# Performance work log

Measured on AMD Instinct MI355X. Metric: run time of the kernel, lower is better.

## Reference

```python
import jax, jax.numpy as jnp
import numpy as np

B, T, N_EMBD, HEAD = 8, 2048, 1024, 64
NEG_INF = -1e30  # stand-in for float('-inf'), safe under fp16/bf16 after where


def setup_inputs() -> dict:
    key = jax.random.key(0)
    k0, k1, k2, k3 = jax.random.split(key, 4)
    idx = jax.random.normal(k0, (B, T, N_EMBD), dtype=jnp.float32)
    # nn.Linear weights have shape (out_features, in_features)
    Wk = jax.random.normal(k1, (HEAD, N_EMBD), dtype=jnp.float32) * 0.02
    Wq = jax.random.normal(k2, (HEAD, N_EMBD), dtype=jnp.float32) * 0.02
    Wv = jax.random.normal(k3, (HEAD, N_EMBD), dtype=jnp.float32) * 0.02
    return {"idx": idx, "Wk": Wk, "Wq": Wq, "Wv": Wv}


def reference(idx, Wk, Wq, Wv):
    # idx: [B,T,C]; W*: [H,C] (torch Linear layout, y = x @ W.T)
    Tn = idx.shape[1]
    k = jnp.einsum('btc,hc->bth', idx, Wk)
    q = jnp.einsum('btc,hc->bth', idx, Wq)
    v = jnp.einsum('btc,hc->bth', idx, Wv)
    # NOTE: original has NO 1/sqrt(head_size) scaling
    wei = jnp.einsum('bth,bsh->bts', q, k)  # [B,T,T]
    causal = jnp.tril(jnp.ones((Tn, Tn), dtype=bool))  # keep where tril != 0
    wei = jnp.where(causal[None, :, :], wei, NEG_INF)
    # NOTE: original softmaxes over dim=1 (query axis), not the last axis
    wei = jax.nn.softmax(wei, axis=1)
    out = jnp.einsum('bts,bsh->bth', wei, v)  # [B,T,H]
    return out
```

## Files before the change

### kernel.cpp

```cpp
#include <hip/hip_runtime.h>


typedef __attribute__((ext_vector_type(8))) short bf16x8;
typedef __attribute__((ext_vector_type(4))) float f32x4;
typedef unsigned short u16;

#define MFMA(a, b, c) __builtin_amdgcn_mfma_f32_16x16x32_bf16((a), (b), (c), 0, 0, 0)

__device__ __forceinline__ u16 f2bf(float x) {
    unsigned u = __float_as_uint(x);
    u += 0x7fff + ((u >> 16) & 1);
    return (u16)(u >> 16);
}
__device__ __forceinline__ float bf2f(u16 h) {
    return __uint_as_float(((unsigned)h) << 16);
}

__device__ __forceinline__ void split8(const f32x4 x0, const f32x4 x1,
                                       bf16x8* hv, bf16x8* lv)
{
    const float f[8] = {x0[0], x0[1], x0[2], x0[3], x1[0], x1[1], x1[2], x1[3]};
    union { unsigned u[4]; bf16x8 v; } H, L;
    #pragma unroll
    for (int j = 0; j < 4; ++j) {
        const unsigned u0 = __float_as_uint(f[2 * j]);
        const unsigned u1 = __float_as_uint(f[2 * j + 1]);
        H.u[j] = __builtin_amdgcn_perm(u1, u0, 0x07060302);
        const float l0 = f[2 * j]     - __uint_as_float(u0 & 0xffff0000u);
        const float l1 = f[2 * j + 1] - __uint_as_float(u1 & 0xffff0000u);
        L.u[j] = __builtin_amdgcn_perm(__float_as_uint(l1), __float_as_uint(l0),
                                       0x07060302);
    }
    *hv = H.v;
    *lv = L.v;
}

typedef const __attribute__((address_space(1))) void* gas_p;
typedef __attribute__((address_space(3))) void* las_p;

#define WH_OFF  0u
#define WL_OFF  (WH_OFF + 192u*1024u*2u)
#define FQH_OFF (WL_OFF + 192u*1024u*2u)
#define FQL_OFF (FQH_OFF + 2u*1024u*1024u)
#define FKH_OFF (FQL_OFF + 2u*1024u*1024u)
#define FKL_OFF (FKH_OFF + 2u*1024u*1024u)
#define VF_OFF  (FKL_OFF + 2u*1024u*1024u)
#define DD_OFF  (VF_OFF + 2u*1024u*1024u)
#define PF_OFF  (DD_OFF + 8u*2048u*4u)

__global__ __launch_bounds__(128) void wsplit_kernel(
    const float* __restrict__ Wk, const float* __restrict__ Wq,
    const float* __restrict__ Wv, u16* __restrict__ FWH)
{
    const int n = blockIdx.x;
    const int nblk = n >> 4, lr = n & 15;
    const float* src = (n < 64) ? (Wq + (long)n * 1024)
                     : (n < 128) ? (Wk + (long)(n - 64) * 1024)
                                 : (Wv + (long)(n - 128) * 1024);
    const int f = threadIdx.x;
    const int kc = f >> 2, q = f & 3;
    const float4 f0 = *(const float4*)&src[kc * 32 + q * 8];
    const float4 f1 = *(const float4*)&src[kc * 32 + q * 8 + 4];
    const float vs[8] = {f0.x, f0.y, f0.z, f0.w, f1.x, f1.y, f1.z, f1.w};
    bf16x8 hv;
    #pragma unroll
    for (int j = 0; j < 8; ++j) hv[j] = (short)f2bf(vs[j]);
    const long o = ((long)(nblk * 32 + kc) * 64 + q * 16 + lr) * 8;
    *(bf16x8*)&FWH[o] = hv;
}

__global__ __launch_bounds__(512, 2) void qkv_kernel(
    const float* __restrict__ idx, const u16* __restrict__ FWH,
    u16* __restrict__ FQH, u16* __restrict__ FQL,
    u16* __restrict__ FKH, u16* __restrict__ VF)
{
    __shared__ __align__(16) char smem[3][40960];
    const int tid = threadIdx.x;
    const int w = tid >> 6, lr = tid & 15, quad = (tid >> 4) & 3;
    const int lane = tid & 63;
    const int r0 = blockIdx.x * 64;
    const int b = r0 >> 11, t0 = r0 & 2047;
    const int m0 = (w & 1) * 32;
    const int nbb = (w >> 1) * 3;

    const float* asrc[2];
    int adst[2];
    #pragma unroll
    for (int j = 0; j < 2; ++j) {
        const int s = w * 2 + j;
        const int row = s * 4 + (lane >> 4);
        const int lc = (lane & 15) ^ (row & 7);
        asrc[j] = idx + (long)(r0 + row) * 1024 + lc * 4;
        adst[j] = s * 1024;
    }
    const u16* fsrc[3];
    int fdst[3];
    #pragma unroll
    for (int j = 0; j < 3; ++j) {
        const int seg = w * 3 + j;
        const int nblk = seg >> 1, kcl = seg & 1;
        fsrc[j] = FWH + (long)nblk * 16384 + kcl * 512 + lane * 8;
        fdst[j] = 16384 + seg * 1024;
    }

#define ISSUE(PH)                                                             \
    {                                                                         \
        const int nb_ = (PH) % 3;                                             \
        _Pragma("unroll")                                                     \
        for (int j = 0; j < 2; ++j)                                           \
            __builtin_amdgcn_global_load_lds((gas_p)(asrc[j] + (PH) * 64),    \
                (las_p)(smem[nb_] + adst[j]), 16, 0, 0);                      \
        _Pragma("unroll")                                                     \
        for (int j = 0; j < 3; ++j)                                           \
            __builtin_amdgcn_global_load_lds((gas_p)(fsrc[j] + (long)(PH) * 1024), \
                (las_p)(smem[nb_] + fdst[j]), 16, 0, 0);                      \
    }

#define COMPUTE(PH)                                                           \
    {                                                                         \
        const int nb_ = (PH) % 3;                                             \
        const float* A_ = (const float*)smem[nb_];                            \
        const u16* F_ = (const u16*)(smem[nb_] + 16384);                      \
        _Pragma("unroll")                                                     \
        for (int kc = 0; kc < 2; ++kc) {                                      \
            bf16x8 AH[2], AL[2];                                              \
            _Pragma("unroll")                                                 \
            for (int mi = 0; mi < 2; ++mi) {                                  \
                const int R = m0 + mi * 16 + lr;                              \
                const int c0 = (kc * 8 + quad * 2) ^ (lr & 7);                \
                const f32x4 x0 = *(const f32x4*)&A_[R * 64 + c0 * 4];         \
                const f32x4 x1 = *(const f32x4*)&A_[R * 64 + (c0 ^ 1) * 4];   \
                split8(x0, x1, &AH[mi], &AL[mi]);                             \
            }                                                                 \
            _Pragma("unroll")                                                 \
            for (int nf = 0; nf < 3; ++nf) {                                  \
                const int sb = (((nbb + nf) * 2 + kc)) * 512 + lane * 8;      \
                const bf16x8 bh = *(const bf16x8*)&F_[sb];                    \
                _Pragma("unroll")                                             \
                for (int mi = 0; mi < 2; ++mi) {                              \
                    f32x4 c = acc[mi][nf];                                    \
                    c = MFMA(AH[mi], bh, c);                                  \
                    c = MFMA(AL[mi], bh, c);                                  \
                    acc[mi][nf] = c;                                          \
                }                                                             \
            }                                                                 \
        }                                                                     \
    }

#define WAITV(N)                                                              \
    asm volatile("s_waitcnt vmcnt(" #N ")" ::: "memory");                     \
    __builtin_amdgcn_sched_barrier(0);                                        \
    __builtin_amdgcn_s_barrier();

    f32x4 acc[2][3] = {};

    ISSUE(0); ISSUE(1);
    WAITV(5)

    for (int ph = 0; ph < 14; ++ph) {
        ISSUE(ph + 2);
        __builtin_amdgcn_sched_barrier(0);
        COMPUTE(ph);
        WAITV(5)
    }
    COMPUTE(14);
    WAITV(0)
    COMPUTE(15);

#undef WAITV
#undef COMPUTE
#undef ISSUE

    #pragma unroll
    for (int mi = 0; mi < 2; ++mi) {
        const int tb = t0 + m0 + mi * 16 + quad * 4;
        const int tblk = (t0 + m0 + mi * 16) >> 4;
        #pragma unroll
        for (int nf = 0; nf < 3; ++nf) {
            const int n = (nbb + nf) * 16 + lr;
            const f32x4 a = acc[mi][nf];
            if (n < 128) {
                const bool isQ = (n < 64);
                const int h = n & 63;
                const int kc = h >> 5;
                const int lsub = 16 * ((h & 31) >> 3);
                const long base = ((long)(b * 128 + tblk) * 2 + kc) * 512 + (h & 7);
                #pragma unroll
                for (int r = 0; r < 4; ++r) {
                    const float v = a[r];
                    const u16 hi = f2bf(v);
                    const long o = base + (long)(quad * 4 + r + lsub) * 8;
                    if (isQ) {
                        FQH[o] = hi;
                        FQL[o] = f2bf(v - bf2f(hi));
                    } else {
                        FKH[o] = hi;
                    }
                }
            } else {
                const int h = n - 128;
                const int hblk = h >> 4;
                #pragma unroll
                for (int r = 0; r < 4; ++r) {
                    const int t = tb + r;
                    const long o = ((long)(b * 4 + hblk) * 64 + (t >> 5)) * 512
                                 + (long)(16 * ((t & 31) >> 3) + (h & 15)) * 8 + (t & 7);
                    VF[o] = f2bf(a[r]);
                }
            }
        }
    }
}

__global__ __launch_bounds__(256, 4) void stats_kernel(
    const u16* __restrict__ FQH, const u16* __restrict__ FQL,
    const u16* __restrict__ FKH,
    u16* __restrict__ PF, float* __restrict__ D)
{
    __shared__ float red[4][64];
    const int tid = threadIdx.x;
    const int w = tid >> 6, lr = tid & 15, quad = (tid >> 4) & 3;
    const int lane = tid & 63;
    const int b = blockIdx.y;
    int x = blockIdx.x, i = 0;
    for (;;) { const int nc = (39 - i) >> 3; if (x < nc) break; x -= nc; ++i; }
    const int s0 = i * 64;
    const int jt0 = i + 8 * x, jt1 = min(jt0 + 8, 32);

    uint2* __restrict__ PQ = (uint2*)PF;

    bf16x8 KH[4][2];
    #pragma unroll
    for (int sf = 0; sf < 4; ++sf) {
        const long kb = ((long)(b * 128 + i * 4 + sf) * 2) * 512 + lane * 8;
        KH[sf][0] = *(const bf16x8*)&FKH[kb];
        KH[sf][1] = *(const bf16x8*)&FKH[kb + 512];
    }

    float dsum[4][4] = {};
    for (int jt = jt0; jt < jt1; ++jt) {
        const long qb = ((long)(b * 128 + jt * 4 + w) * 2) * 512 + lane * 8;
        const bf16x8 qh0 = *(const bf16x8*)&FQH[qb];
        const bf16x8 qh1 = *(const bf16x8*)&FQH[qb + 512];
        const bf16x8 ql0 = *(const bf16x8*)&FQL[qb];
        const bf16x8 ql1 = *(const bf16x8*)&FQL[qb + 512];
        const bool diag = (jt == i);
        const int t_sub = w * 16 + lr;
        const long tb_base = ((long)(b * 128 + jt * 4 + w)) * 512;
        #pragma unroll
        for (int sf = 0; sf < 4; ++sf) {
            f32x4 cc = {};
            cc = MFMA(KH[sf][0], qh0, cc);
            cc = MFMA(KH[sf][0], ql0, cc);
            cc = MFMA(KH[sf][1], qh1, cc);
            cc = MFMA(KH[sf][1], ql1, cc);

            u16 hq[4];
            #pragma unroll
            for (int r = 0; r < 4; ++r) {
                float ev = __expf(cc[r]);
                if (diag && (t_sub < sf * 16 + quad * 4 + r)) ev = 0.f;
                dsum[sf][r] += ev;
                hq[r] = f2bf(ev);
            }
            uint2 pk;
            pk.x = (unsigned)hq[0] | ((unsigned)hq[1] << 16);
            pk.y = (unsigned)hq[2] | ((unsigned)hq[3] << 16);
            PQ[(tb_base + i * 16 + sf * 4 + quad) * 16 + lr] = pk;
        }
    }

    #pragma unroll
    for (int sf = 0; sf < 4; ++sf)
        #pragma unroll
        for (int r = 0; r < 4; ++r) {
            float v = dsum[sf][r];
            v += __shfl_xor(v, 1);
            v += __shfl_xor(v, 2);
            v += __shfl_xor(v, 4);
            v += __shfl_xor(v, 8);
            dsum[sf][r] = v;
        }
    if (lr == 0) {
        #pragma unroll
        for (int sf = 0; sf < 4; ++sf)
            #pragma unroll
            for (int r = 0; r < 4; ++r)
                red[w][sf * 16 + quad * 4 + r] = dsum[sf][r];
    }
    __syncthreads();
    if (tid < 64)
        atomicAdd(&D[b * 2048 + s0 + tid],
                  red[0][tid] + red[1][tid] + red[2][tid] + red[3][tid]);
}

__global__ __launch_bounds__(256) void vscale_kernel(
    u16* __restrict__ VF, const float* __restrict__ D)
{
    const int g = blockIdx.x * 256 + threadIdx.x;
    const long e = (long)g * 8;
    const int lane = (int)((e >> 3) & 63);
    const int kc   = (int)((e >> 9) & 63);
    const int b    = (int)(e >> 17);
    const int s = kc * 32 + (lane >> 4) * 8;
    const float4 d0 = *(const float4*)&D[b * 2048 + s];
    const float4 d1 = *(const float4*)&D[b * 2048 + s + 4];
    const float dv[8] = {d0.x, d0.y, d0.z, d0.w, d1.x, d1.y, d1.z, d1.w};
    bf16x8 vv = *(bf16x8*)&VF[e];
    bf16x8 ov;
    #pragma unroll
    for (int j = 0; j < 8; ++j)
        ov[j] = (short)f2bf(bf2f((u16)vv[j]) / dv[j]);
    *(bf16x8*)&VF[e] = ov;
}

__global__ __launch_bounds__(256, 4) void out_kernel(
    const u16* __restrict__ PF, const u16* __restrict__ VF,
    float* __restrict__ out)
{
    const int tid = threadIdx.x;
    const int w = tid >> 6, lr = tid & 15, quad = (tid >> 4) & 3;
    const int lane = tid & 63;
    const int b = blockIdx.y;
    int x = blockIdx.x, i = 0;
    for (;;) { const int nc = (i + 8) >> 3; if (x < nc) break; x -= nc; ++i; }
    const int t0 = i * 64;
    const int js0 = 8 * x, js1 = min(8 * x + 8, i + 1);
    const int tblk = i * 4 + w;

    const uint2* __restrict__ PQ = (const uint2*)PF;
    const int g = lane >> 4, tr = lane & 15;
    const long tb_base = ((long)(b * 128 + tblk)) * 512;

    f32x4 oacc[4] = {};
    for (int js = js0; js < js1; ++js) {
        bf16x8 pa[2];
        #pragma unroll
        for (int kcp = 0; kcp < 2; ++kcp) {
            const long u = (tb_base + js * 16 + kcp * 8 + g * 2) * 16 + tr;
            const uint2 a0 = PQ[u];
            const uint2 a1 = PQ[u + 16];
            union { unsigned uu[4]; bf16x8 v; } P_;
            P_.uu[0] = a0.x; P_.uu[1] = a0.y; P_.uu[2] = a1.x; P_.uu[3] = a1.y;
            pa[kcp] = P_.v;
        }
        #pragma unroll
        for (int nf = 0; nf < 4; ++nf) {
            const long vb = ((long)(b * 4 + nf) * 64 + 2 * js) * 512 + lane * 8;
            const bf16x8 v0 = *(const bf16x8*)&VF[vb];
            const bf16x8 v1 = *(const bf16x8*)&VF[vb + 512];
            oacc[nf] = MFMA(pa[0], v0, oacc[nf]);
            oacc[nf] = MFMA(pa[1], v1, oacc[nf]);
        }
    }

    const bool single = (i < 8);
    #pragma unroll
    for (int nf = 0; nf < 4; ++nf) {
        const int h = nf * 16 + lr;
        #pragma unroll
        for (int r = 0; r < 4; ++r) {
            const int t = t0 + w * 16 + quad * 4 + r;
            const long o = (long)(b * 2048 + t) * 64 + h;
            if (single) out[o] = oacc[nf][r];
            else        atomicAdd(&out[o], oacc[nf][r]);
        }
    }
}

extern "C" void kernel_launch(void* const* d_in, const int* in_sizes, int n_in,
                              void* d_out, int out_size, void* d_ws, size_t ws_size,
                              hipStream_t stream)
{
    const float* idx = (const float*)d_in[0];
    const float* Wk  = (const float*)d_in[1];
    const float* Wq  = (const float*)d_in[2];
    const float* Wv  = (const float*)d_in[3];
    char* ws = (char*)d_ws;
    float* out = (float*)d_out;

    u16* FWH = (u16*)(ws + WH_OFF);
    u16* FQH = (u16*)(ws + FQH_OFF); u16* FQL = (u16*)(ws + FQL_OFF);
    u16* FKH = (u16*)(ws + FKH_OFF);
    u16* VF  = (u16*)(ws + VF_OFF);
    float* Dp = (float*)(ws + DD_OFF);
    u16* PF  = (u16*)(ws + PF_OFF);

    hipMemsetAsync(out, 0, (size_t)8 * 2048 * 64 * sizeof(float), stream);
    hipMemsetAsync(Dp, 0, (size_t)8 * 2048 * sizeof(float), stream);

    wsplit_kernel<<<192, 128, 0, stream>>>(Wk, Wq, Wv, FWH);
    qkv_kernel<<<256, 512, 0, stream>>>(idx, FWH, FQH, FQL, FKH, VF);
    stats_kernel<<<dim3(80, 8), 256, 0, stream>>>(FQH, FQL, FKH, PF, Dp);
    vscale_kernel<<<512, 256, 0, stream>>>(VF, Dp);
    out_kernel<<<dim3(80, 8), 256, 0, stream>>>(PF, VF, out);
}
```

Measured before the change: 145.9 us.

## Drop Q low-part split and fold column-sum normalization into output kernel

Removes the hi/lo bf16 split of Q, so the score computation uses two MFMAs per tile instead of four and no longer writes or reads the FQL buffer. It also deletes the separate vscale kernel that divided V by the column sums. That division now happens in out_kernel, where each P element is multiplied by the reciprocal of its column sum before the MFMA. The intent is to save one kernel launch plus memory traffic and matrix work. In exchange, the scores lose precision because Q is now a single bf16 value, and with no 1/sqrt scaling the exponent amplifies that error, so accuracy may suffer. The normalization also uses an approximate reciprocal.

```diff
diff --git a/kernel.cpp b/kernel.cpp
--- a/kernel.cpp
+++ b/kernel.cpp
@@ -71,8 +71,7 @@
 
 __global__ __launch_bounds__(512, 2) void qkv_kernel(
     const float* __restrict__ idx, const u16* __restrict__ FWH,
-    u16* __restrict__ FQH, u16* __restrict__ FQL,
-    u16* __restrict__ FKH, u16* __restrict__ VF)
+    u16* __restrict__ FQH, u16* __restrict__ FKH, u16* __restrict__ VF)
 {
     __shared__ __align__(16) char smem[3][40960];
     const int tid = threadIdx.x;
@@ -180,22 +179,15 @@
             const int n = (nbb + nf) * 16 + lr;
             const f32x4 a = acc[mi][nf];
             if (n < 128) {
-                const bool isQ = (n < 64);
+                u16* Hd = (n < 64) ? FQH : FKH;
                 const int h = n & 63;
                 const int kc = h >> 5;
                 const int lsub = 16 * ((h & 31) >> 3);
                 const long base = ((long)(b * 128 + tblk) * 2 + kc) * 512 + (h & 7);
                 #pragma unroll
                 for (int r = 0; r < 4; ++r) {
-                    const float v = a[r];
-                    const u16 hi = f2bf(v);
                     const long o = base + (long)(quad * 4 + r + lsub) * 8;
-                    if (isQ) {
-                        FQH[o] = hi;
-                        FQL[o] = f2bf(v - bf2f(hi));
-                    } else {
-                        FKH[o] = hi;
-                    }
+                    Hd[o] = f2bf(a[r]);
                 }
             } else {
                 const int h = n - 128;
@@ -213,8 +205,7 @@
 }
 
 __global__ __launch_bounds__(256, 4) void stats_kernel(
-    const u16* __restrict__ FQH, const u16* __restrict__ FQL,
-    const u16* __restrict__ FKH,
+    const u16* __restrict__ FQH, const u16* __restrict__ FKH,
     u16* __restrict__ PF, float* __restrict__ D)
 {
     __shared__ float red[4][64];
@@ -242,8 +233,6 @@
         const long qb = ((long)(b * 128 + jt * 4 + w) * 2) * 512 + lane * 8;
         const bf16x8 qh0 = *(const bf16x8*)&FQH[qb];
         const bf16x8 qh1 = *(const bf16x8*)&FQH[qb + 512];
-        const bf16x8 ql0 = *(const bf16x8*)&FQL[qb];
-        const bf16x8 ql1 = *(const bf16x8*)&FQL[qb + 512];
         const bool diag = (jt == i);
         const int t_sub = w * 16 + lr;
         const long tb_base = ((long)(b * 128 + jt * 4 + w)) * 512;
@@ -251,9 +240,7 @@
         for (int sf = 0; sf < 4; ++sf) {
             f32x4 cc = {};
             cc = MFMA(KH[sf][0], qh0, cc);
-            cc = MFMA(KH[sf][0], ql0, cc);
             cc = MFMA(KH[sf][1], qh1, cc);
-            cc = MFMA(KH[sf][1], ql1, cc);
 
             u16 hq[4];
             #pragma unroll
@@ -294,29 +281,9 @@
                   red[0][tid] + red[1][tid] + red[2][tid] + red[3][tid]);
 }
 
-__global__ __launch_bounds__(256) void vscale_kernel(
-    u16* __restrict__ VF, const float* __restrict__ D)
-{
-    const int g = blockIdx.x * 256 + threadIdx.x;
-    const long e = (long)g * 8;
-    const int lane = (int)((e >> 3) & 63);
-    const int kc   = (int)((e >> 9) & 63);
-    const int b    = (int)(e >> 17);
-    const int s = kc * 32 + (lane >> 4) * 8;
-    const float4 d0 = *(const float4*)&D[b * 2048 + s];
-    const float4 d1 = *(const float4*)&D[b * 2048 + s + 4];
-    const float dv[8] = {d0.x, d0.y, d0.z, d0.w, d1.x, d1.y, d1.z, d1.w};
-    bf16x8 vv = *(bf16x8*)&VF[e];
-    bf16x8 ov;
-    #pragma unroll
-    for (int j = 0; j < 8; ++j)
-        ov[j] = (short)f2bf(bf2f((u16)vv[j]) / dv[j]);
-    *(bf16x8*)&VF[e] = ov;
-}
-
 __global__ __launch_bounds__(256, 4) void out_kernel(
     const u16* __restrict__ PF, const u16* __restrict__ VF,
-    float* __restrict__ out)
+    const float* __restrict__ D, float* __restrict__ out)
 {
     const int tid = threadIdx.x;
     const int w = tid >> 6, lr = tid & 15, quad = (tid >> 4) & 3;
@@ -342,7 +309,16 @@
             const uint2 a1 = PQ[u + 16];
             union { unsigned uu[4]; bf16x8 v; } P_;
             P_.uu[0] = a0.x; P_.uu[1] = a0.y; P_.uu[2] = a1.x; P_.uu[3] = a1.y;
-            pa[kcp] = P_.v;
+            const int sb = js * 64 + kcp * 32 + g * 8;
+            const float4 d0 = *(const float4*)&D[b * 2048 + sb];
+            const float4 d1 = *(const float4*)&D[b * 2048 + sb + 4];
+            const float dv[8] = {d0.x, d0.y, d0.z, d0.w, d1.x, d1.y, d1.z, d1.w};
+            bf16x8 sc;
+            #pragma unroll
+            for (int j = 0; j < 8; ++j)
+                sc[j] = (short)f2bf(bf2f((u16)P_.v[j]) *
+                                    __builtin_amdgcn_rcpf(dv[j]));
+            pa[kcp] = sc;
         }
         #pragma unroll
         for (int nf = 0; nf < 4; ++nf) {
@@ -380,7 +356,7 @@
     float* out = (float*)d_out;
 
     u16* FWH = (u16*)(ws + WH_OFF);
-    u16* FQH = (u16*)(ws + FQH_OFF); u16* FQL = (u16*)(ws + FQL_OFF);
+    u16* FQH = (u16*)(ws + FQH_OFF);
     u16* FKH = (u16*)(ws + FKH_OFF);
     u16* VF  = (u16*)(ws + VF_OFF);
     float* Dp = (float*)(ws + DD_OFF);
@@ -390,8 +366,7 @@
     hipMemsetAsync(Dp, 0, (size_t)8 * 2048 * sizeof(float), stream);
 
     wsplit_kernel<<<192, 128, 0, stream>>>(Wk, Wq, Wv, FWH);
-    qkv_kernel<<<256, 512, 0, stream>>>(idx, FWH, FQH, FQL, FKH, VF);
-    stats_kernel<<<dim3(80, 8), 256, 0, stream>>>(FQH, FQL, FKH, PF, Dp);
-    vscale_kernel<<<512, 256, 0, stream>>>(VF, Dp);
-    out_kernel<<<dim3(80, 8), 256, 0, stream>>>(PF, VF, out);
-}
+    qkv_kernel<<<256, 512, 0, stream>>>(idx, FWH, FQH, FKH, VF);
+    stats_kernel<<<dim3(80, 8), 256, 0, stream>>>(FQH, FKH, PF, Dp);
+    out_kernel<<<dim3(80, 8), 256, 0, stream>>>(PF, VF, Dp, out);
+}
```

Measured after the change: 142.8 us. 2.1% less time.
